# Optimization experiments

Hardware: AMD Instinct MI355X
Metric: run time of the kernel (lower is better)

The kernel has to match this reference:

```python
import jax, jax.numpy as jnp
import numpy as np

N_NODES = 100000
N_EDGES = 640000
D_IN = 128
D_HID = 128
D_OUT = 64


def gcn_conv(x, src, dst, ew, W, b, num_nodes):
    """GCNConv with add_self_loops=False: h = D^{-1/2} A D^{-1/2} (x W) + b.

    PyG gcn_norm: row, col = edge_index; deg = scatter_add(edge_weight, col);
    norm = deg^{-1/2}[row] * ew * deg^{-1/2}[col]; aggregate messages into col.
    """
    h = x @ W  # [N, d_out]
    deg = jax.ops.segment_sum(ew, dst, num_segments=num_nodes)  # [N]
    dinv = jnp.where(deg > 0, jax.lax.rsqrt(deg), 0.0)
    norm = dinv[src] * ew * dinv[dst]  # [E]
    out = jax.ops.segment_sum(norm[:, None] * h[src], dst, num_segments=num_nodes)
    return out + b


def setup_inputs() -> dict:
    key = jax.random.key(0)
    ks = jax.random.split(key, 9)
    x = jax.random.normal(ks[0], (N_NODES, D_IN), dtype=jnp.float32)
    edge_index = jax.random.randint(ks[1], (2, N_EDGES), 0, N_NODES, dtype=jnp.int64)
    edge_weight = jax.random.uniform(ks[2], (N_EDGES,), dtype=jnp.float32)
    def glorot(k, fan_in, fan_out):
        s = jnp.sqrt(6.0 / (fan_in + fan_out))
        return jax.random.uniform(k, (fan_in, fan_out), minval=-s, maxval=s, dtype=jnp.float32)
    W1 = glorot(ks[3], D_IN, D_HID); b1 = jnp.zeros((D_HID,), jnp.float32)
    W2 = glorot(ks[4], D_HID, D_HID); b2 = jnp.zeros((D_HID,), jnp.float32)
    W3 = glorot(ks[5], D_HID, D_OUT); b3 = jnp.zeros((D_OUT,), jnp.float32)
    return {"x": x, "edge_index": edge_index, "edge_weight": edge_weight,
            "W1": W1, "b1": b1, "W2": W2, "b2": b2, "W3": W3, "b3": b3}


def reference(x, edge_index, edge_weight, W1, b1, W2, b2, W3, b3):
    src, dst = edge_index[0], edge_index[1]
    n = x.shape[0]
    embeddings = []
    h = gcn_conv(x, src, dst, edge_weight, W1, b1, n)
    h = jax.nn.relu(h)
    embeddings.append(h)
    h = gcn_conv(h, src, dst, edge_weight, W2, b2, n)
    h = jax.nn.relu(h)
    embeddings.append(h)
    h = gcn_conv(h, src, dst, edge_weight, W3, b3, n)
    embeddings.append(h)
    return tuple(embeddings)
```

## Files before the change

### kernel.cpp

```cpp
#include <hip/hip_runtime.h>

#define NN 100000
#define NE 640000
#define GB1 ((NN + 63) / 64)
#define EPB ((NE + GB1 - 1) / GB1)
#define PWB 160
#define ZB  ((2 * NN + 255) / 256)

typedef unsigned int uint32;
typedef unsigned long long uint64;
typedef __attribute__((ext_vector_type(8))) short short8;
typedef __attribute__((ext_vector_type(4))) float f32x4;

static __device__ __forceinline__ ushort f2bf(float f) {
    uint32 u = __float_as_uint(f);
    u = (u + 0x7fffu + ((u >> 16) & 1u)) >> 16;
    return (ushort)u;
}
static __device__ __forceinline__ float bf2f(uint32 bits16) {
    return __uint_as_float(bits16 << 16);
}
static __device__ __forceinline__ uint32 pack2(float a, float b) {
    return (uint32)f2bf(a) | ((uint32)f2bf(b) << 16);
}

__global__ void k_prep_zero(const float* __restrict__ W1, const float* __restrict__ W2,
                            const float* __restrict__ W3, ushort* __restrict__ wt1,
                            ushort* __restrict__ wt2, ushort* __restrict__ wt3,
                            int* __restrict__ degcnt_i) {
    const int b = blockIdx.x;
    if (b < PWB) {
        int o = b * 256 + threadIdx.x;
        if (o < 16384) {
            int col = o >> 7, k = o & 127;
            wt1[o] = f2bf(W1[k * 128 + col]);
        } else if (o < 32768) {
            int oo = o - 16384;
            int col = oo >> 7, k = oo & 127;
            wt2[oo] = f2bf(W2[k * 128 + col]);
        } else if (o < 40960) {
            int oo = o - 32768;
            int col = oo >> 7, k = oo & 127;
            wt3[oo] = f2bf(W3[k * 64 + col]);
        }
    } else {
        int i = (b - PWB) * 256 + threadIdx.x;
        if (i < 2 * NN) degcnt_i[i] = 0;
    }
}

template <int NOUT>
static __device__ __forceinline__ void gemm_body(const float* __restrict__ X,
                                                 const ushort* __restrict__ Wt,
                                                 ushort* __restrict__ H, int N,
                                                 int bid, int tid, char* smem) {
    char* xs = smem;
    char* wt = smem + 64 * 256;
    const int row0 = bid * 64;

    const uint4* Wt4 = reinterpret_cast<const uint4*>(Wt);
#pragma unroll
    for (int i = 0; i < NOUT / 16; ++i) {
        int id = tid + 256 * i;
        int col = id >> 4, c4 = id & 15;
        uint4 v = Wt4[id];
        *reinterpret_cast<uint4*>(wt + col * 256 + ((c4 * 16) ^ ((col & 7) << 4))) = v;
    }
#pragma unroll
    for (int i = 0; i < 8; ++i) {
        int id = tid + 256 * i;
        int r = id >> 5, c4 = id & 31;
        int gr = row0 + r;
        float4 v = make_float4(0.f, 0.f, 0.f, 0.f);
        if (gr < N) v = *reinterpret_cast<const float4*>(&X[(size_t)gr * 128 + c4 * 4]);
        uint2 pk;
        pk.x = pack2(v.x, v.y);
        pk.y = pack2(v.z, v.w);
        *reinterpret_cast<uint2*>(xs + r * 256 + ((c4 * 8) ^ ((r & 7) << 4))) = pk;
    }
    __syncthreads();

    const int w = tid >> 6, lane = tid & 63;
    const int rl = w * 16 + (lane & 15);
    const int kg = lane >> 4;
    f32x4 acc[NOUT / 16];
#pragma unroll
    for (int ct = 0; ct < NOUT / 16; ++ct) acc[ct] = (f32x4){0.f, 0.f, 0.f, 0.f};

#pragma unroll
    for (int ks = 0; ks < 4; ++ks) {
        const int kb = ks * 64 + kg * 16;
        short8 a = *reinterpret_cast<const short8*>(xs + rl * 256 + (kb ^ ((rl & 7) << 4)));
#pragma unroll
        for (int ct = 0; ct < NOUT / 16; ++ct) {
            int col = ct * 16 + (lane & 15);
            short8 bfr = *reinterpret_cast<const short8*>(wt + col * 256 + (kb ^ ((col & 7) << 4)));
            acc[ct] = __builtin_amdgcn_mfma_f32_16x16x32_bf16(a, bfr, acc[ct], 0, 0, 0);
        }
    }
#pragma unroll
    for (int ct = 0; ct < NOUT / 16; ++ct) {
        int col = ct * 16 + (lane & 15);
#pragma unroll
        for (int r = 0; r < 4; ++r) {
            int gr = row0 + w * 16 + (lane >> 4) * 4 + r;
            if (gr < N) H[(size_t)gr * NOUT + col] = f2bf(acc[ct][r]);
        }
    }
}

__global__ __launch_bounds__(256) void k_gemm1_hist(const float* __restrict__ X,
                                                    const ushort* __restrict__ Wt1,
                                                    ushort* __restrict__ H, int N,
                                                    const int* __restrict__ dst,
                                                    const float* __restrict__ ew,
                                                    uint64* __restrict__ degcnt) {
    __shared__ char smem[64 * 256 + 128 * 256];
    gemm_body<128>(X, Wt1, H, N, blockIdx.x, threadIdx.x, smem);
    const int ebase = blockIdx.x * EPB;
    const int eend = (ebase + EPB < NE) ? ebase + EPB : NE;
    for (int e = ebase + threadIdx.x; e < eend; e += 256) {
        uint64 pk = (1ull << 44) | (uint64)(ew[e] * 4294967296.0f);
        atomicAdd(&degcnt[dst[e]], pk);
    }
}

template <int NOUT>
__global__ __launch_bounds__(256) void k_gemm_mfma(const float* __restrict__ X,
                                                   const ushort* __restrict__ Wt,
                                                   ushort* __restrict__ H, int N) {
    __shared__ char smem[64 * 256 + NOUT * 256];
    gemm_body<NOUT>(X, Wt, H, N, blockIdx.x, threadIdx.x, smem);
}


__global__ void k_scan1(const uint64* __restrict__ degcnt, int* __restrict__ rp,
                        int* __restrict__ bsum, int n) {
    __shared__ int tsum[256];
    const int base = blockIdx.x * 1024;
    const int t = threadIdx.x;
    int v[4], s = 0;
#pragma unroll
    for (int j = 0; j < 4; ++j) {
        int idx = base + t * 4 + j;
        v[j] = (idx < n) ? (int)(degcnt[idx] >> 44) : 0;
        s += v[j];
    }
    tsum[t] = s;
    __syncthreads();
    for (int off = 1; off < 256; off <<= 1) {
        int x = (t >= off) ? tsum[t - off] : 0;
        __syncthreads();
        tsum[t] += x;
        __syncthreads();
    }
    int excl = (t > 0) ? tsum[t - 1] : 0;
#pragma unroll
    for (int j = 0; j < 4; ++j) {
        int idx = base + t * 4 + j;
        if (idx < n) rp[idx] = excl;
        excl += v[j];
    }
    if (t == 255) bsum[blockIdx.x] = tsum[255];
}

__global__ void k_scan2(int* __restrict__ bsum, int nb) {
    __shared__ int sh[256];
    int t = threadIdx.x;
    sh[t] = (t < nb) ? bsum[t] : 0;
    __syncthreads();
    for (int off = 1; off < 256; off <<= 1) {
        int x = (t >= off) ? sh[t - off] : 0;
        __syncthreads();
        sh[t] += x;
        __syncthreads();
    }
    if (t < nb) bsum[t] = (t > 0) ? sh[t - 1] : 0;
}

__global__ void k_scan3(int* __restrict__ rp, const int* __restrict__ bsum,
                        int* __restrict__ cursor, const uint64* __restrict__ degcnt,
                        float* __restrict__ dinv, int n) {
    int i = blockIdx.x * blockDim.x + threadIdx.x;
    if (i < n) {
        int v = rp[i] + bsum[i >> 10];
        rp[i] = v;
        cursor[i] = v;
        float d = (float)(degcnt[i] & 0xFFFFFFFFFFFull) * (1.0f / 4294967296.0f);
        dinv[i] = (d > 0.f) ? rsqrtf(d) : 0.f;
    }
    if (i == 0) rp[n] = NE;
}

__global__ void k_fill(const int* __restrict__ src, const int* __restrict__ dst,
                       const float* __restrict__ ew, const float* __restrict__ dinv,
                       int* __restrict__ cursor, uint2* __restrict__ ep, int E) {
    int e = blockIdx.x * blockDim.x + threadIdx.x;
    if (e < E) {
        int s = src[e], d = dst[e];
        int pos = atomicAdd(&cursor[d], 1);
        float nv = dinv[s] * ew[e] * dinv[d];
        ep[pos] = make_uint2((uint32)s, __float_as_uint(nv));
    }
}

template <int WAVES, int RELU>
__global__ void k_agg128(const int* __restrict__ rp, const uint2* __restrict__ ep,
                         const ushort* __restrict__ H, const float* __restrict__ b,
                         float* __restrict__ out, int N) {
    const int wave = threadIdx.x >> 6;
    const int lane = threadIdx.x & 63;
    const int n = blockIdx.x * WAVES + wave;
    if (n >= N) return;
    const int e0 = rp[n], e1 = rp[n + 1];
    const int slot = lane >> 4;
    const int l16 = lane & 15;

    const float4 b0 = *reinterpret_cast<const float4*>(&b[l16 * 8]);
    const float4 b1 = *reinterpret_cast<const float4*>(&b[l16 * 8 + 4]);

    float a[8] = {};
    int e = e0 + slot;
    if (e < e1) {
        uint2 p = ep[e];
        for (;;) {
            const int en = e + 4;
            uint2 pn = ep[en];
            float w = __uint_as_float(p.y);
            uint4 hv = *reinterpret_cast<const uint4*>(&H[(size_t)p.x * 128 + l16 * 8]);
            a[0] = fmaf(w, bf2f(hv.x & 0xffffu), a[0]);
            a[1] = fmaf(w, bf2f(hv.x >> 16), a[1]);
            a[2] = fmaf(w, bf2f(hv.y & 0xffffu), a[2]);
            a[3] = fmaf(w, bf2f(hv.y >> 16), a[3]);
            a[4] = fmaf(w, bf2f(hv.z & 0xffffu), a[4]);
            a[5] = fmaf(w, bf2f(hv.z >> 16), a[5]);
            a[6] = fmaf(w, bf2f(hv.w & 0xffffu), a[6]);
            a[7] = fmaf(w, bf2f(hv.w >> 16), a[7]);
            e = en;
            if (e >= e1) break;
            p = pn;
        }
    }
#pragma unroll
    for (int j = 0; j < 8; ++j) {
        a[j] += __shfl_xor(a[j], 32);
        a[j] += __shfl_xor(a[j], 16);
    }
    if (lane < 16) {
        float4 o0 = make_float4(a[0] + b0.x, a[1] + b0.y, a[2] + b0.z, a[3] + b0.w);
        float4 o1 = make_float4(a[4] + b1.x, a[5] + b1.y, a[6] + b1.z, a[7] + b1.w);
        if (RELU) {
            o0.x = fmaxf(o0.x, 0.f); o0.y = fmaxf(o0.y, 0.f);
            o0.z = fmaxf(o0.z, 0.f); o0.w = fmaxf(o0.w, 0.f);
            o1.x = fmaxf(o1.x, 0.f); o1.y = fmaxf(o1.y, 0.f);
            o1.z = fmaxf(o1.z, 0.f); o1.w = fmaxf(o1.w, 0.f);
        }
        float* op = &out[(size_t)n * 128 + l16 * 8];
        *reinterpret_cast<float4*>(op) = o0;
        *reinterpret_cast<float4*>(op + 4) = o1;
    }
}

template <int WAVES, int RELU>
__global__ void k_agg64(const int* __restrict__ rp, const uint2* __restrict__ ep,
                        const ushort* __restrict__ H, const float* __restrict__ b,
                        float* __restrict__ out, int N) {
    const int wave = threadIdx.x >> 6;
    const int lane = threadIdx.x & 63;
    const int n = blockIdx.x * WAVES + wave;
    if (n >= N) return;
    const int e0 = rp[n], e1 = rp[n + 1];
    const int slot = lane >> 3;
    const int l8 = lane & 7;

    const float4 b0 = *reinterpret_cast<const float4*>(&b[l8 * 8]);
    const float4 b1 = *reinterpret_cast<const float4*>(&b[l8 * 8 + 4]);

    float a[8] = {};
    int e = e0 + slot;
    if (e < e1) {
        uint2 p = ep[e];
        for (;;) {
            const int en = e + 8;
            uint2 pn = ep[en];
            float w = __uint_as_float(p.y);
            uint4 hv = *reinterpret_cast<const uint4*>(&H[(size_t)p.x * 64 + l8 * 8]);
            a[0] = fmaf(w, bf2f(hv.x & 0xffffu), a[0]);
            a[1] = fmaf(w, bf2f(hv.x >> 16), a[1]);
            a[2] = fmaf(w, bf2f(hv.y & 0xffffu), a[2]);
            a[3] = fmaf(w, bf2f(hv.y >> 16), a[3]);
            a[4] = fmaf(w, bf2f(hv.z & 0xffffu), a[4]);
            a[5] = fmaf(w, bf2f(hv.z >> 16), a[5]);
            a[6] = fmaf(w, bf2f(hv.w & 0xffffu), a[6]);
            a[7] = fmaf(w, bf2f(hv.w >> 16), a[7]);
            e = en;
            if (e >= e1) break;
            p = pn;
        }
    }
#pragma unroll
    for (int j = 0; j < 8; ++j) {
        a[j] += __shfl_xor(a[j], 8);
        a[j] += __shfl_xor(a[j], 16);
        a[j] += __shfl_xor(a[j], 32);
    }
    if (lane < 8) {
        float4 o0 = make_float4(a[0] + b0.x, a[1] + b0.y, a[2] + b0.z, a[3] + b0.w);
        float4 o1 = make_float4(a[4] + b1.x, a[5] + b1.y, a[6] + b1.z, a[7] + b1.w);
        if (RELU) {
            o0.x = fmaxf(o0.x, 0.f); o0.y = fmaxf(o0.y, 0.f);
            o0.z = fmaxf(o0.z, 0.f); o0.w = fmaxf(o0.w, 0.f);
            o1.x = fmaxf(o1.x, 0.f); o1.y = fmaxf(o1.y, 0.f);
            o1.z = fmaxf(o1.z, 0.f); o1.w = fmaxf(o1.w, 0.f);
        }
        float* op = &out[(size_t)n * 64 + l8 * 8];
        *reinterpret_cast<float4*>(op) = o0;
        *reinterpret_cast<float4*>(op + 4) = o1;
    }
}


extern "C" void kernel_launch(void* const* d_in, const int* in_sizes, int n_in,
                              void* d_out, int out_size, void* d_ws, size_t ws_size,
                              hipStream_t stream) {
    const float* x  = (const float*)d_in[0];
    const int*   ei = (const int*)d_in[1];
    const float* ew = (const float*)d_in[2];
    const float* W1 = (const float*)d_in[3];
    const float* b1 = (const float*)d_in[4];
    const float* W2 = (const float*)d_in[5];
    const float* b2 = (const float*)d_in[6];
    const float* W3 = (const float*)d_in[7];
    const float* b3 = (const float*)d_in[8];

    const int* src = ei;
    const int* dst = ei + NE;

    float*  ws     = (float*)d_ws;
    uint64* degcnt = (uint64*)ws;
    int*    rp     = (int*)(ws + 2 * NN);
    int*    bsum   = (int*)(ws + 3 * NN + 64);
    uint2*  ep     = (uint2*)(ws + 3 * NN + 256);
    ushort* h1     = (ushort*)(ws + 3 * NN + 256 + 2 * NE);
    ushort* h2     = h1 + (size_t)NN * 128;
    ushort* h3     = h1;
    ushort* wt1    = h2 + (size_t)NN * 128;
    ushort* wt2    = wt1 + 128 * 128;
    ushort* wt3    = wt2 + 128 * 128;
    int*    cursor = (int*)h2;

    float* out0 = (float*)d_out;
    float* out1 = out0 + NN * 128;
    float* out2 = out1 + NN * 128;
    float* dinv = out2;

    const int B = 256;
    const int NB_SCAN = (NN + 1023) / 1024;

    k_prep_zero<<<PWB + ZB, B, 0, stream>>>(W1, W2, W3, wt1, wt2, wt3, (int*)degcnt);

    k_gemm1_hist<<<GB1, 256, 0, stream>>>(x, wt1, h1, NN, dst, ew, degcnt);

    k_scan1<<<NB_SCAN, 256, 0, stream>>>(degcnt, rp, bsum, NN);
    k_scan2<<<1, 256, 0, stream>>>(bsum, NB_SCAN);
    k_scan3<<<(NN + B - 1) / B, B, 0, stream>>>(rp, bsum, cursor, degcnt, dinv, NN);
    k_fill<<<(NE + B - 1) / B, B, 0, stream>>>(src, dst, ew, dinv, cursor, ep, NE);

    k_agg128<4, 1><<<(NN + 3) / 4, 256, 0, stream>>>(rp, ep, h1, b1, out0, NN);

    k_gemm_mfma<128><<<GB1, 256, 0, stream>>>(out0, wt2, h2, NN);
    k_agg128<4, 1><<<(NN + 3) / 4, 256, 0, stream>>>(rp, ep, h2, b2, out1, NN);

    k_gemm_mfma<64><<<GB1, 256, 0, stream>>>(out1, wt3, h3, NN);
    k_agg64<4, 0><<<(NN + 3) / 4, 256, 0, stream>>>(rp, ep, h3, b3, out2, NN);
}
```

Before: 239.3 us.

## Replace three-pass scan with single-pass atomic block-offset scan and explicit row ends

Fuses the block scan, block-sum scan and offset fixup into one kernel. Each block claims its output base by atomically adding its total to a global counter, so segments are placed in arbitrary block order. To stay correct, the kernel stores a separate end offset per node, and the aggregation kernels read start and end arrays instead of adjacent row pointers. This removes two kernel launches and a pass over the row pointers, at the cost of one extra int array and non-monotonic edge layout across blocks.

```diff
diff --git a/kernel.cpp b/kernel.cpp
--- a/kernel.cpp
+++ b/kernel.cpp
@@ -5,7 +5,7 @@
 #define GB1 ((NN + 63) / 64)
 #define EPB ((NE + GB1 - 1) / GB1)
 #define PWB 160
-#define ZB  ((2 * NN + 255) / 256)
+#define ZB  ((2 * NN + 64 + 255) / 256)
 
 typedef unsigned int uint32;
 typedef unsigned long long uint64;
@@ -27,7 +27,7 @@
 __global__ void k_prep_zero(const float* __restrict__ W1, const float* __restrict__ W2,
                             const float* __restrict__ W3, ushort* __restrict__ wt1,
                             ushort* __restrict__ wt2, ushort* __restrict__ wt3,
-                            int* __restrict__ degcnt_i) {
+                            int* __restrict__ zbase) {
     const int b = blockIdx.x;
     if (b < PWB) {
         int o = b * 256 + threadIdx.x;
@@ -45,7 +45,7 @@
         }
     } else {
         int i = (b - PWB) * 256 + threadIdx.x;
-        if (i < 2 * NN) degcnt_i[i] = 0;
+        if (i < 2 * NN + 64) zbase[i] = 0;
     }
 }
 
@@ -133,17 +133,20 @@
     gemm_body<NOUT>(X, Wt, H, N, blockIdx.x, threadIdx.x, smem);
 }
 
-
-__global__ void k_scan1(const uint64* __restrict__ degcnt, int* __restrict__ rp,
-                        int* __restrict__ bsum, int n) {
+__global__ void k_scan(const uint64* __restrict__ degcnt, int* __restrict__ rp,
+                       int* __restrict__ rpe, int* __restrict__ cursor,
+                       float* __restrict__ dinv, int* __restrict__ base_ctr, int n) {
     __shared__ int tsum[256];
+    __shared__ int sbase;
     const int base = blockIdx.x * 1024;
     const int t = threadIdx.x;
     int v[4], s = 0;
+    uint64 dc[4];
 #pragma unroll
     for (int j = 0; j < 4; ++j) {
         int idx = base + t * 4 + j;
-        v[j] = (idx < n) ? (int)(degcnt[idx] >> 44) : 0;
+        dc[j] = (idx < n) ? degcnt[idx] : 0ull;
+        v[j] = (int)(dc[j] >> 44);
         s += v[j];
     }
     tsum[t] = s;
@@ -154,42 +157,21 @@
         tsum[t] += x;
         __syncthreads();
     }
-    int excl = (t > 0) ? tsum[t - 1] : 0;
+    if (t == 255) sbase = atomicAdd(base_ctr, tsum[255]);
+    __syncthreads();
+    int excl = sbase + ((t > 0) ? tsum[t - 1] : 0);
 #pragma unroll
     for (int j = 0; j < 4; ++j) {
         int idx = base + t * 4 + j;
-        if (idx < n) rp[idx] = excl;
+        if (idx < n) {
+            rp[idx] = excl;
+            rpe[idx] = excl + v[j];
+            cursor[idx] = excl;
+            float d = (float)(dc[j] & 0xFFFFFFFFFFFull) * (1.0f / 4294967296.0f);
+            dinv[idx] = (d > 0.f) ? rsqrtf(d) : 0.f;
+        }
         excl += v[j];
     }
-    if (t == 255) bsum[blockIdx.x] = tsum[255];
-}
-
-__global__ void k_scan2(int* __restrict__ bsum, int nb) {
-    __shared__ int sh[256];
-    int t = threadIdx.x;
-    sh[t] = (t < nb) ? bsum[t] : 0;
-    __syncthreads();
-    for (int off = 1; off < 256; off <<= 1) {
-        int x = (t >= off) ? sh[t - off] : 0;
-        __syncthreads();
-        sh[t] += x;
-        __syncthreads();
-    }
-    if (t < nb) bsum[t] = (t > 0) ? sh[t - 1] : 0;
-}
-
-__global__ void k_scan3(int* __restrict__ rp, const int* __restrict__ bsum,
-                        int* __restrict__ cursor, const uint64* __restrict__ degcnt,
-                        float* __restrict__ dinv, int n) {
-    int i = blockIdx.x * blockDim.x + threadIdx.x;
-    if (i < n) {
-        int v = rp[i] + bsum[i >> 10];
-        rp[i] = v;
-        cursor[i] = v;
-        float d = (float)(degcnt[i] & 0xFFFFFFFFFFFull) * (1.0f / 4294967296.0f);
-        dinv[i] = (d > 0.f) ? rsqrtf(d) : 0.f;
-    }
-    if (i == 0) rp[n] = NE;
 }
 
 __global__ void k_fill(const int* __restrict__ src, const int* __restrict__ dst,
@@ -205,14 +187,14 @@
 }
 
 template <int WAVES, int RELU>
-__global__ void k_agg128(const int* __restrict__ rp, const uint2* __restrict__ ep,
-                         const ushort* __restrict__ H, const float* __restrict__ b,
-                         float* __restrict__ out, int N) {
+__global__ void k_agg128(const int* __restrict__ rp, const int* __restrict__ rpe,
+                         const uint2* __restrict__ ep, const ushort* __restrict__ H,
+                         const float* __restrict__ b, float* __restrict__ out, int N) {
     const int wave = threadIdx.x >> 6;
     const int lane = threadIdx.x & 63;
     const int n = blockIdx.x * WAVES + wave;
     if (n >= N) return;
-    const int e0 = rp[n], e1 = rp[n + 1];
+    const int e0 = rp[n], e1 = rpe[n];
     const int slot = lane >> 4;
     const int l16 = lane & 15;
 
@@ -262,14 +244,14 @@
 }
 
 template <int WAVES, int RELU>
-__global__ void k_agg64(const int* __restrict__ rp, const uint2* __restrict__ ep,
-                        const ushort* __restrict__ H, const float* __restrict__ b,
-                        float* __restrict__ out, int N) {
+__global__ void k_agg64(const int* __restrict__ rp, const int* __restrict__ rpe,
+                        const uint2* __restrict__ ep, const ushort* __restrict__ H,
+                        const float* __restrict__ b, float* __restrict__ out, int N) {
     const int wave = threadIdx.x >> 6;
     const int lane = threadIdx.x & 63;
     const int n = blockIdx.x * WAVES + wave;
     if (n >= N) return;
-    const int e0 = rp[n], e1 = rp[n + 1];
+    const int e0 = rp[n], e1 = rpe[n];
     const int slot = lane >> 3;
     const int l8 = lane & 7;
 
@@ -336,18 +318,19 @@
     const int* src = ei;
     const int* dst = ei + NE;
 
-    float*  ws     = (float*)d_ws;
-    uint64* degcnt = (uint64*)ws;
-    int*    rp     = (int*)(ws + 2 * NN);
-    int*    bsum   = (int*)(ws + 3 * NN + 64);
-    uint2*  ep     = (uint2*)(ws + 3 * NN + 256);
-    ushort* h1     = (ushort*)(ws + 3 * NN + 256 + 2 * NE);
-    ushort* h2     = h1 + (size_t)NN * 128;
-    ushort* h3     = h1;
-    ushort* wt1    = h2 + (size_t)NN * 128;
-    ushort* wt2    = wt1 + 128 * 128;
-    ushort* wt3    = wt2 + 128 * 128;
-    int*    cursor = (int*)h2;
+    float*  ws       = (float*)d_ws;
+    uint64* degcnt   = (uint64*)ws;
+    int*    base_ctr = (int*)(ws + 2 * NN);
+    int*    rp       = (int*)(ws + 2 * NN + 64);
+    int*    rpe      = (int*)(ws + 3 * NN + 64);
+    uint2*  ep       = (uint2*)(ws + 4 * NN + 128);
+    ushort* h1       = (ushort*)(ws + 4 * NN + 128 + 2 * NE);
+    ushort* h2       = h1 + (size_t)NN * 128;
+    ushort* h3       = h1;
+    ushort* wt1      = h2 + (size_t)NN * 128;
+    ushort* wt2      = wt1 + 128 * 128;
+    ushort* wt3      = wt2 + 128 * 128;
+    int*    cursor   = (int*)h2;
 
     float* out0 = (float*)d_out;
     float* out1 = out0 + NN * 128;
@@ -361,16 +344,14 @@
 
     k_gemm1_hist<<<GB1, 256, 0, stream>>>(x, wt1, h1, NN, dst, ew, degcnt);
 
-    k_scan1<<<NB_SCAN, 256, 0, stream>>>(degcnt, rp, bsum, NN);
-    k_scan2<<<1, 256, 0, stream>>>(bsum, NB_SCAN);
-    k_scan3<<<(NN + B - 1) / B, B, 0, stream>>>(rp, bsum, cursor, degcnt, dinv, NN);
+    k_scan<<<NB_SCAN, 256, 0, stream>>>(degcnt, rp, rpe, cursor, dinv, base_ctr, NN);
     k_fill<<<(NE + B - 1) / B, B, 0, stream>>>(src, dst, ew, dinv, cursor, ep, NE);
 
-    k_agg128<4, 1><<<(NN + 3) / 4, 256, 0, stream>>>(rp, ep, h1, b1, out0, NN);
+    k_agg128<4, 1><<<(NN + 3) / 4, 256, 0, stream>>>(rp, rpe, ep, h1, b1, out0, NN);
 
     k_gemm_mfma<128><<<GB1, 256, 0, stream>>>(out0, wt2, h2, NN);
-    k_agg128<4, 1><<<(NN + 3) / 4, 256, 0, stream>>>(rp, ep, h2, b2, out1, NN);
+    k_agg128<4, 1><<<(NN + 3) / 4, 256, 0, stream>>>(rp, rpe, ep, h2, b2, out1, NN);
 
     k_gemm_mfma<64><<<GB1, 256, 0, stream>>>(out1, wt3, h3, NN);
-    k_agg64<4, 0><<<(NN + 3) / 4, 256, 0, stream>>>(rp, ep, h3, b3, out2, NN);
-}
+    k_agg64<4, 0><<<(NN + 3) / 4, 256, 0, stream>>>(rp, rpe, ep, h3, b3, out2, NN);
+}
```

Measured after the change: 235.0 us. No clear change (-1.8%).
